# Kernel optimization log

Hardware: AMD Instinct MI355X
Metric: run time of the kernel (lower is better)

## Reference

```python
import jax, jax.numpy as jnp
import numpy as np

HID = 2048      # hidden_size
NH = 16         # num_attention_heads
QLR = 1536      # q_lora_rank
KVLR = 512      # kv_lora_rank
DN = 128        # qk_nope_head_dim
DR = 64         # qk_rope_head_dim
DQK = DN + DR   # qk_head_dim = 192
DV = 128        # v_head_dim
EPS = 1e-6
THETA = 10000.0
B, T = 2, 2048


def rmsnorm(x, scale):
    return x * jax.lax.rsqrt(jnp.mean(x * x, axis=-1, keepdims=True) + EPS) * scale


def rope(x, positions):
    # x: [B, T, h, d]; NeoX-style rotate-half RoPE on the rope slice only
    d = x.shape[-1]
    inv_freq = 1.0 / (THETA ** (jnp.arange(0, d, 2, dtype=jnp.float32) / d))
    ang = positions.astype(jnp.float32)[..., None] * inv_freq       # [B, T, d/2]
    cos = jnp.cos(ang)[:, :, None, :]
    sin = jnp.sin(ang)[:, :, None, :]
    x1, x2 = jnp.split(x, 2, axis=-1)
    return jnp.concatenate([x1 * cos - x2 * sin, x2 * cos + x1 * sin], axis=-1).astype(x.dtype)


def setup_inputs() -> dict:
    key = jax.random.key(0)
    ks = jax.random.split(key, 8)
    s = 0.02
    x = jax.random.normal(ks[0], (B, T, HID), dtype=jnp.float32)
    attention_mask = jnp.ones((B, T), dtype=bool)
    positions = jnp.broadcast_to(jnp.arange(T, dtype=jnp.int32), (B, T))
    wqa = jax.random.normal(ks[1], (HID, QLR), dtype=jnp.float32) * s
    qa_scale = jnp.ones((QLR,), dtype=jnp.float32)
    wqb = jax.random.normal(ks[2], (QLR, NH * DQK), dtype=jnp.float32) * s
    wkva = jax.random.normal(ks[3], (HID, KVLR + DR), dtype=jnp.float32) * s
    kva_scale = jnp.ones((KVLR,), dtype=jnp.float32)
    wkvb = jax.random.normal(ks[4], (KVLR, NH * (DN + DV)), dtype=jnp.float32) * s
    wo = jax.random.normal(ks[5], (NH * DV, HID), dtype=jnp.float32) * s
    return {"x": x, "attention_mask": attention_mask, "positions": positions,
            "wqa": wqa, "qa_scale": qa_scale, "wqb": wqb,
            "wkva": wkva, "kva_scale": kva_scale, "wkvb": wkvb, "wo": wo}


def reference(x, attention_mask, positions, wqa, qa_scale, wqb, wkva, kva_scale, wkvb, wo):
    Bv, Tv, _ = x.shape
    # low-rank Q: hid -> q_lora_rank -> rmsnorm -> heads*qk_head_dim
    q = (rmsnorm(x @ wqa, qa_scale) @ wqb).reshape(Bv, Tv, NH, DQK)
    q_pass, q_rot = q[..., :DN], q[..., DN:]
    # compressed KV + shared rope key
    ckv = x @ wkva                                    # [B, T, KVLR + DR]
    kv_lat, k_rot = ckv[..., :KVLR], ckv[..., KVLR:].reshape(Bv, Tv, 1, DR)
    kv = (rmsnorm(kv_lat, kva_scale) @ wkvb).reshape(Bv, Tv, NH, DN + DV)
    k_pass, v = kv[..., :DN], kv[..., DN:]
    # decoupled RoPE on rope slice only
    q_rot = rope(q_rot, positions)
    k_rot = jnp.broadcast_to(rope(k_rot, positions), (Bv, Tv, NH, DR))
    q = jnp.concatenate([q_pass, q_rot], axis=-1)     # [B, T, H, 192]
    k = jnp.concatenate([k_pass, k_rot], axis=-1)
    # masked causal SDPA; v padding in the original is a no-op mathematically
    scale = DQK ** -0.5
    scores = jnp.einsum('bqhd,bkhd->bhqk', q, k) * scale
    causal = jnp.tril(jnp.ones((Tv, Tv), dtype=bool))
    mask = causal[None, None, :, :] & attention_mask[:, None, None, :].astype(bool)
    scores = jnp.where(mask, scores, jnp.finfo(scores.dtype).min)
    probs = jax.nn.softmax(scores, axis=-1)
    out = jnp.einsum('bhqk,bkhd->bqhd', probs, v).reshape(Bv, Tv, NH * DV)
    return out @ wo
```

## Files before the change

kernel.cpp:

```cpp
#include <hip/hip_runtime.h>
#include <math.h>
#include <stdint.h>

#define NHEAD 16
#define HIDDIM 2048
#define QLRANK 1536
#define KVRANK 512
#define DROT 64
#define BB 2
#define TT 2048
#define BTOK (BB*TT)
#define NPROJ 2304
#define CKV0 1536
#define ROT0 2048

typedef __bf16 bf16x8 __attribute__((ext_vector_type(8)));
typedef __bf16 bf16x4 __attribute__((ext_vector_type(4)));
typedef float f32x4 __attribute__((ext_vector_type(4)));
typedef uint16_t u16;
typedef uint32_t u32;

__device__ __forceinline__ u16 f2bf(float f) {
  union { float f; uint32_t u; } v; v.f = f;
  uint32_t r = v.u + 0x7fffu + ((v.u >> 16) & 1u);
  return (u16)(r >> 16);
}
__device__ __forceinline__ float bf2f(u16 h) {
  union { uint32_t u; float f; } v; v.u = ((uint32_t)h) << 16;
  return v.f;
}

__device__ __forceinline__ void gload_lds16(const u16* g, u16* l) {
  __builtin_amdgcn_global_load_lds(
      (const __attribute__((address_space(1))) uint32_t*)g,
      (__attribute__((address_space(3))) uint32_t*)l, 16, 0, 0);
}

__global__ __launch_bounds__(256) void cvt_f32_bf16(const float* __restrict__ in,
                                                    u16* __restrict__ out, int n) {
  int idx = (blockIdx.x * 256 + threadIdx.x) * 8;
  if (idx >= n) return;
  f32x4 a = *(const f32x4*)&in[idx];
  f32x4 b = *(const f32x4*)&in[idx + 4];
  union { f32x4 q; u16 e[8]; } w;
#pragma unroll
  for (int j = 0; j < 4; ++j) { w.e[j] = f2bf(a[j]); w.e[4 + j] = f2bf(b[j]); }
  *(f32x4*)&out[idx] = w.q;
}

__global__ __launch_bounds__(256) void transpose_w(const float* __restrict__ W,
                                                   u16* __restrict__ Wt,
                                                   int K, int N, int Npad, float scale,
                                                   const float* __restrict__ svec) {
  __shared__ float tile[32][33];
  int k0 = blockIdx.x * 32, n0 = blockIdx.y * 32;
  int tx = threadIdx.x, ty = threadIdx.y;
#pragma unroll
  for (int r = 0; r < 32; r += 8) {
    int k = k0 + ty + r, n = n0 + tx;
    tile[ty + r][tx] = (k < K && n < N) ? W[(size_t)k * N + n] : 0.f;
  }
  __syncthreads();
  float sv = scale * (svec ? svec[k0 + tx] : 1.f);
#pragma unroll
  for (int r = 0; r < 32; r += 8) {
    int n = n0 + ty + r, k = k0 + tx;
    if (n < Npad && k < K) Wt[(size_t)n * K + k] = f2bf(tile[tx][ty + r] * sv);
  }
}

template<int D>
__global__ __launch_bounds__(256) void row_invrms(const u16* __restrict__ in, int stride,
                                                  float* __restrict__ out) {
  const int row = blockIdx.x;
  const int tid = threadIdx.x;
  constexpr int NC = D / 8;
  float ss = 0.f;
  if (tid < NC) {
    union { f32x4 q; u16 e[8]; } t;
    t.q = *(const f32x4*)&in[(size_t)row * stride + tid * 8];
#pragma unroll
    for (int j = 0; j < 8; ++j) { float v = bf2f(t.e[j]); ss += v * v; }
  }
#pragma unroll
  for (int off = 1; off < 64; off <<= 1) ss += __shfl_xor(ss, off);
  __shared__ float red[4];
  if ((tid & 63) == 0) red[tid >> 6] = ss;
  __syncthreads();
  if (tid == 0)
    out[row] = rsqrtf((red[0] + red[1] + red[2] + red[3]) / (float)D + 1e-6f);
}

template<int OUTF32>
__global__ __launch_bounds__(256) void gemm_bt(const u16* __restrict__ A, int lda,
                                               const u16* __restrict__ Bt,
                                               void* __restrict__ Cv, int ldc,
                                               const float* __restrict__ rowscale,
                                               int N, int K) {
  __shared__ __align__(16) u16 As[2][128 * 32];
  __shared__ __align__(16) u16 Bs[2][128 * 32];
  const int tid = threadIdx.x;
  const int lane = tid & 63;
  const int wave = tid >> 6;
  const int bm = blockIdx.y * 128;
  const int bn = blockIdx.x * 128;
  const int wr = wave >> 1;
  const int wc = wave & 1;

  f32x4 acc[4][4] = {};

  const int srow = wave * 16 + (lane >> 2);
  const int scol = (lane & 3) * 8;
  const u16* Ag = A + (size_t)(bm + srow) * lda + scol;
  const u16* Bg = Bt + (size_t)(bn + srow) * K + scol;
  const int soff = (wave * 16) * 32;

  const int a_off = (wr * 64 + (lane & 15)) * 32 + (lane >> 4) * 8;
  const int b_off = (wc * 64 + (lane & 15)) * 32 + (lane >> 4) * 8;

  const int nt = K >> 5;

  gload_lds16(Ag, &As[0][soff]);
  gload_lds16(Ag + (size_t)64 * lda, &As[0][soff + 64 * 32]);
  gload_lds16(Bg, &Bs[0][soff]);
  gload_lds16(Bg + (size_t)64 * K, &Bs[0][soff + 64 * 32]);
  __syncthreads();

  int cur = 0;
  for (int t = 0; t < nt; ++t) {
    if (t + 1 < nt) {
      const int k0 = (t + 1) << 5;
      gload_lds16(Ag + k0, &As[cur ^ 1][soff]);
      gload_lds16(Ag + (size_t)64 * lda + k0, &As[cur ^ 1][soff + 64 * 32]);
      gload_lds16(Bg + k0, &Bs[cur ^ 1][soff]);
      gload_lds16(Bg + (size_t)64 * K + k0, &Bs[cur ^ 1][soff + 64 * 32]);
    }
    bf16x8 af[4], bfr[4];
#pragma unroll
    for (int m = 0; m < 4; ++m) af[m] = *(const bf16x8*)&As[cur][a_off + m * 16 * 32];
#pragma unroll
    for (int n = 0; n < 4; ++n) bfr[n] = *(const bf16x8*)&Bs[cur][b_off + n * 16 * 32];
#pragma unroll
    for (int m = 0; m < 4; ++m)
#pragma unroll
      for (int n = 0; n < 4; ++n)
        acc[m][n] = __builtin_amdgcn_mfma_f32_16x16x32_bf16(af[m], bfr[n], acc[m][n], 0, 0, 0);
    if (t + 1 < nt) {
      __syncthreads();
      cur ^= 1;
    }
  }

  const int row0 = bm + wr * 64 + (lane >> 4) * 4;
  const int col0 = bn + wc * 64 + (lane & 15);
#pragma unroll
  for (int m = 0; m < 4; ++m) {
    float rs[4] = {1.f, 1.f, 1.f, 1.f};
    if (rowscale) {
#pragma unroll
      for (int i = 0; i < 4; ++i) rs[i] = rowscale[row0 + m * 16 + i];
    }
#pragma unroll
    for (int n = 0; n < 4; ++n)
#pragma unroll
      for (int i = 0; i < 4; ++i) {
        size_t idx = (size_t)(row0 + m * 16 + i) * ldc + (col0 + n * 16);
        float v = acc[m][n][i] * rs[i];
        if (OUTF32) ((float*)Cv)[idx] = v;
        else        ((u16*)Cv)[idx] = f2bf(v);
      }
  }
}

template<int OUTF32>
__global__ __launch_bounds__(512, 2) void gemm256(const u16* __restrict__ A, int lda,
                                                  const u16* __restrict__ Bt,
                                                  void* __restrict__ Cv, int ldc,
                                                  const float* __restrict__ rowscale,
                                                  int K) {
  __shared__ __align__(16) u16 S[2][2][16384];
  const int tid = threadIdx.x, lane = tid & 63, wave = tid >> 6;
  const int l15 = lane & 15, l4 = lane >> 4;
  const int bm = blockIdx.y * 256, bn = blockIdx.x * 256;
  const int wm = wave >> 2, wn = wave & 3;

  const int rlo = lane >> 3;
  const int cbase = (((lane & 7) ^ (rlo & 7)) * 8);
  const u16* src[8];
  u16* dst[8];
#pragma unroll
  for (int j = 0; j < 8; ++j) {
    int gj = wave * 8 + j;
    if (gj < 32) {
      src[j] = A + (size_t)(bm + gj * 8 + rlo) * lda + cbase;
      dst[j] = &S[0][0][0] + gj * 512;
    } else {
      src[j] = Bt + (size_t)(bn + (gj - 32) * 8 + rlo) * K + cbase;
      dst[j] = &S[0][1][0] + (gj - 32) * 512;
    }
  }

  const int r7 = l15 & 7;
  const int acol = (l4 ^ r7) * 16;
  const char* Sa0 = (const char*)&S[0][0][0] + wm * 16384;
  const char* Sb0 = (const char*)&S[0][1][0] + (wn >> 1) * 16384;
  const int arow0 = l15 * 128;
  const int brow0 = ((wn & 1) * 64 + l15) * 128;

  f32x4 acc[8][4] = {};
  const int nt = K >> 6;

#pragma unroll
  for (int j = 0; j < 8; ++j) gload_lds16(src[j], dst[j]);
#pragma unroll
  for (int j = 0; j < 8; ++j) gload_lds16(src[j] + 64, dst[j] + 32768);
  asm volatile("s_waitcnt vmcnt(8)" ::: "memory");
  __builtin_amdgcn_s_barrier();
  __builtin_amdgcn_sched_barrier(0);

  for (int t = 0; t < nt; ++t) {
    const char* Sab = Sa0 + (t & 1) * 65536;
    const char* Sbb = Sb0 + (t & 1) * 65536;
    bf16x8 bfr[4][2];
#pragma unroll
    for (int fn = 0; fn < 4; ++fn) {
      bfr[fn][0] = *(const bf16x8*)(Sbb + brow0 + fn * 2048 + acol);
      bfr[fn][1] = *(const bf16x8*)(Sbb + brow0 + fn * 2048 + (acol ^ 64));
    }
#pragma unroll
    for (int q = 0; q < 4; ++q) {
      bf16x8 a0[2], a1[2];
#pragma unroll
      for (int m2 = 0; m2 < 2; ++m2) {
        const int fm = q * 2 + m2;
        a0[m2] = *(const bf16x8*)(Sab + arow0 + fm * 2048 + acol);
        a1[m2] = *(const bf16x8*)(Sab + arow0 + fm * 2048 + (acol ^ 64));
      }
      __builtin_amdgcn_s_setprio(1);
#pragma unroll
      for (int m2 = 0; m2 < 2; ++m2)
#pragma unroll
        for (int fn = 0; fn < 4; ++fn) {
          f32x4 c = acc[q * 2 + m2][fn];
          c = __builtin_amdgcn_mfma_f32_16x16x32_bf16(a0[m2], bfr[fn][0], c, 0, 0, 0);
          c = __builtin_amdgcn_mfma_f32_16x16x32_bf16(a1[m2], bfr[fn][1], c, 0, 0, 0);
          acc[q * 2 + m2][fn] = c;
        }
      __builtin_amdgcn_s_setprio(0);
    }
    if (t + 1 < nt) {
      __builtin_amdgcn_s_barrier();
      __builtin_amdgcn_sched_barrier(0);
      if (t + 2 < nt) {
        const int koff = (t + 2) * 64;
#pragma unroll
        for (int j = 0; j < 8; ++j) gload_lds16(src[j] + koff, dst[j] + (t & 1) * 32768);
        asm volatile("s_waitcnt vmcnt(8)" ::: "memory");
      } else {
        asm volatile("s_waitcnt vmcnt(0)" ::: "memory");
      }
      __builtin_amdgcn_s_barrier();
      __builtin_amdgcn_sched_barrier(0);
    }
  }

  const int row0 = bm + wm * 128 + l4 * 4;
  const int col0 = bn + wn * 64 + l15;
#pragma unroll
  for (int fm = 0; fm < 8; ++fm) {
    float rs[4] = {1.f, 1.f, 1.f, 1.f};
    if (rowscale) {
#pragma unroll
      for (int i = 0; i < 4; ++i) rs[i] = rowscale[row0 + fm * 16 + i];
    }
#pragma unroll
    for (int fn = 0; fn < 4; ++fn)
#pragma unroll
      for (int i = 0; i < 4; ++i) {
        size_t idx = (size_t)(row0 + fm * 16 + i) * ldc + (col0 + fn * 16);
        float v = acc[fm][fn][i] * rs[i];
        if (OUTF32) ((float*)Cv)[idx] = v;
        else        ((u16*)Cv)[idx] = f2bf(v);
      }
  }
}

__global__ __launch_bounds__(256) void rope_table(const int* __restrict__ positions,
                                                  float2* __restrict__ tab) {
  int idx = blockIdx.x * 256 + threadIdx.x;
  if (idx >= BTOK * 32) return;
  int bt = idx >> 5, i = idx & 31;
  float invf = powf(10000.0f, -(float)i / 32.0f);
  float ang = (float)positions[bt] * invf;
  tab[idx] = make_float2(cosf(ang), sinf(ang));
}

__global__ __launch_bounds__(256) void rope_q(u16* __restrict__ q,
                                              const float2* __restrict__ tab) {
  int idx = blockIdx.x * 256 + threadIdx.x;
  if (idx >= BTOK * NHEAD * 32) return;
  int i = idx & 31;
  int h = (idx >> 5) & 15;
  int bt = idx >> 9;
  u16* p = q + (size_t)bt * 3072 + h * 192 + 128;
  float x1 = bf2f(p[i]), x2 = bf2f(p[32 + i]);
  float2 cs = tab[bt * 32 + i];
  p[i] = f2bf(x1 * cs.x - x2 * cs.y);
  p[32 + i] = f2bf(x2 * cs.x + x1 * cs.y);
}

__global__ __launch_bounds__(256) void assemble_k(const u16* __restrict__ kv,
                                                  const u16* __restrict__ proj,
                                                  const float2* __restrict__ tab,
                                                  u16* __restrict__ kf) {
  int bt = blockIdx.x;
  __shared__ __align__(16) u16 krot[64];
  int t = threadIdx.x;
  if (t < 64) {
    int i = t & 31;
    float2 cs = tab[bt * 32 + i];
    float x1 = bf2f(proj[(size_t)bt * NPROJ + ROT0 + i]);
    float x2 = bf2f(proj[(size_t)bt * NPROJ + ROT0 + 32 + i]);
    krot[t] = f2bf((t < 32) ? (x1 * cs.x - x2 * cs.y) : (x2 * cs.x + x1 * cs.y));
  }
  __syncthreads();
  for (int c = t; c < 16 * 24; c += 256) {
    int h = c / 24, seg = c % 24;
    u16* dst = kf + (size_t)bt * 3072 + h * 192 + seg * 8;
    if (seg < 16)
      *(f32x4*)dst = *(const f32x4*)&kv[(size_t)bt * 4096 + h * 256 + seg * 8];
    else
      *(f32x4*)dst = *(const f32x4*)&krot[(seg - 16) * 8];
  }
}

__device__ const int8_t JOB_QT[24] = {15,15,7,14,14,13,13,6,12,12,11,11,5,10,10,9,9,4,8,8,3,2,1,0};
__device__ const int8_t JOB_PC[24] = { 0, 1,2, 0, 1, 0, 1,2, 0, 1, 0, 1,2, 0, 1,0,1,2,0,1,2,2,2,2};

__global__ __launch_bounds__(256, 2) void attn_fwd6(const u16* __restrict__ Q,
                                                    const u16* __restrict__ Kf,
                                                    const u16* __restrict__ KV,
                                                    u16* __restrict__ O,
                                                    u16* __restrict__ Opart,
                                                    float2* __restrict__ ml) {
  __shared__ __align__(16) u16 Ks[64 * 192];
  __shared__ __align__(16) u16 Vs[64 * 128];
  __shared__ __align__(16) u16 Ps[4][32][72];

  const int tid = threadIdx.x, lane = tid & 63, wave = tid >> 6;
  const int l15 = lane & 15, l4 = lane >> 4;
  const int jobrank = blockIdx.x >> 5;
  const int bh = blockIdx.x & 31;
  const int qt = JOB_QT[jobrank];
  const int piece = JOB_PC[jobrank];
  const int q0 = qt * 128;
  const int b = bh >> 4, h = bh & 15;
  const int wq0 = q0 + wave * 32;

  bf16x8 qf[2][6];
#pragma unroll
  for (int m = 0; m < 2; ++m) {
    const u16* qp = Q + (size_t)(b * TT + wq0 + m * 16 + l15) * 3072 + h * 192 + l4 * 8;
#pragma unroll
    for (int kk = 0; kk < 6; ++kk) qf[m][kk] = *(const bf16x8*)(qp + kk * 32);
  }

  int ksrc[6];
#pragma unroll
  for (int j = 0; j < 6; ++j) {
    int o = (wave * 6 + j) * 1024 + lane * 16;
    int row = o / 384, col = o % 384;
    int scol = col ^ ((row & 7) << 4);
    ksrc[j] = row * 3072 + (scol >> 1);
  }
  int vsrc[4];
#pragma unroll
  for (int j = 0; j < 4; ++j) {
    int lam = (wave * 4 + j) * 512 + lane * 8;
    int kap = ((lam >> 6) & 15) * 4 + ((lam >> 4) & 3);
    int key = ((kap >> 5) & 1) * 32 + ((kap >> 2) & 3) * 8 + ((kap >> 4) & 1) * 4 + (kap & 3);
    int dv  = (lam >> 10) * 16 + (lam & 15);
    vsrc[j] = key * 4096 + dv;
  }
  const u16* Kbase = Kf + (size_t)(b * TT) * 3072 + h * 192;
  const u16* Vbase = KV + (size_t)(b * TT) * 4096 + h * 256 + 128;
  u16* KsW = Ks + (wave * 6) * 512;
  u16* VsW = Vs + (wave * 4) * 512;
  const unsigned vs_base = (unsigned)(uintptr_t)(&Vs[0]);

  f32x4 o_acc[2][8] = {};
  float m_r[2], l_r[2];
#pragma unroll
  for (int m = 0; m < 2; ++m) { m_r[m] = -INFINITY; l_r[m] = 0.f; }

  const int kt0 = (piece == 1) ? (qt + 1) : 0;
  const int kt1 = (piece == 0) ? (qt + 1) : (2 * qt + 2);

  for (int kt = kt0; kt < kt1; ++kt) {
    __syncthreads();
    const u16* Kt = Kbase + (size_t)(kt * 64) * 3072;
    const u16* Vt = Vbase + (size_t)(kt * 64) * 4096;
#pragma unroll
    for (int j = 0; j < 6; ++j) gload_lds16(Kt + ksrc[j], KsW + j * 512);
#pragma unroll
    for (int j = 0; j < 4; ++j) gload_lds16(Vt + vsrc[j], VsW + j * 512);
    __syncthreads();

    if (kt * 64 > wq0 + 31) continue;
    const int kt64 = kt * 64;

    f32x4 s[2][4] = {};
    __builtin_amdgcn_s_setprio(1);
#pragma unroll
    for (int n = 0; n < 4; ++n) {
      const int krow = n * 16 + l15;
      const int swz = (l15 & 7) << 3;
#pragma unroll
      for (int kk = 0; kk < 6; ++kk) {
        bf16x8 kb = *(const bf16x8*)&Ks[krow * 192 + ((kk * 32 + l4 * 8) ^ swz)];
        s[0][n] = __builtin_amdgcn_mfma_f32_16x16x32_bf16(kb, qf[0][kk], s[0][n], 0, 0, 0);
        s[1][n] = __builtin_amdgcn_mfma_f32_16x16x32_bf16(kb, qf[1][kk], s[1][n], 0, 0, 0);
      }
    }
    __builtin_amdgcn_s_setprio(0);

#pragma unroll
    for (int m = 0; m < 2; ++m) {
      const int qrow = wq0 + m * 16 + l15;
      const bool needmask = (kt64 + 63) > (wq0 + m * 16);
      if (needmask) {
#pragma unroll
        for (int n = 0; n < 4; ++n)
#pragma unroll
          for (int i = 0; i < 4; ++i)
            if (kt64 + n * 16 + l4 * 4 + i > qrow) s[m][n][i] = -INFINITY;
      }
      float pmax = -INFINITY;
#pragma unroll
      for (int n = 0; n < 4; ++n)
#pragma unroll
        for (int i = 0; i < 4; ++i) pmax = fmaxf(pmax, s[m][n][i]);
      pmax = fmaxf(pmax, __shfl_xor(pmax, 16));
      pmax = fmaxf(pmax, __shfl_xor(pmax, 32));

      if (!__all(pmax - m_r[m] <= 8.f)) {
        float mn = fmaxf(m_r[m], pmax);
        float alpha = __expf(m_r[m] - mn);
        m_r[m] = mn;
        l_r[m] *= alpha;
        float ab[4];
#pragma unroll
        for (int i = 0; i < 4; ++i) ab[i] = __shfl(alpha, l4 * 4 + i);
#pragma unroll
        for (int n = 0; n < 8; ++n)
#pragma unroll
          for (int i = 0; i < 4; ++i) o_acc[m][n][i] *= ab[i];
      }

      float psum = 0.f;
#pragma unroll
      for (int n = 0; n < 4; ++n) {
        float p0 = __expf(s[m][n][0] - m_r[m]);
        float p1 = __expf(s[m][n][1] - m_r[m]);
        float p2 = __expf(s[m][n][2] - m_r[m]);
        float p3 = __expf(s[m][n][3] - m_r[m]);
        psum += (p0 + p1) + (p2 + p3);
        union { uint2 d; u16 e[4]; } pw;
        pw.e[0] = f2bf(p0); pw.e[1] = f2bf(p1);
        pw.e[2] = f2bf(p2); pw.e[3] = f2bf(p3);
        *(uint2*)&Ps[wave][m * 16 + l15][n * 16 + l4 * 4] = pw.d;
      }
      psum += __shfl_xor(psum, 16);
      psum += __shfl_xor(psum, 32);
      l_r[m] += psum;
    }

    asm volatile("s_waitcnt lgkmcnt(0)" ::: "memory");
    __builtin_amdgcn_sched_barrier(0);

#pragma unroll
    for (int kk = 0; kk < 2; ++kk) {
      bf16x8 pa[2];
      pa[0] = *(const bf16x8*)&Ps[wave][l15][kk * 32 + l4 * 8];
      pa[1] = *(const bf16x8*)&Ps[wave][16 + l15][kk * 32 + l4 * 8];
      const unsigned va = vs_base + kk * 1024 + lane * 8;
#pragma unroll
      for (int g = 0; g < 2; ++g) {
        union { uint2 u; bf16x4 b; } lo[4], hi[4];
#pragma unroll
        for (int n = 0; n < 4; ++n) {
          unsigned a0 = va + (g * 4 + n) * 2048;
          asm volatile("ds_read_b64_tr_b16 %0, %1" : "=v"(lo[n].u) : "v"(a0));
          asm volatile("ds_read_b64_tr_b16 %0, %1 offset:512" : "=v"(hi[n].u) : "v"(a0));
        }
        asm volatile("s_waitcnt lgkmcnt(0)" ::: "memory");
        __builtin_amdgcn_sched_barrier(0);
        __builtin_amdgcn_s_setprio(1);
#pragma unroll
        for (int n = 0; n < 4; ++n) {
          bf16x8 vb = __builtin_shufflevector(lo[n].b, hi[n].b, 0, 1, 2, 3, 4, 5, 6, 7);
          o_acc[0][g * 4 + n] = __builtin_amdgcn_mfma_f32_16x16x32_bf16(pa[0], vb, o_acc[0][g * 4 + n], 0, 0, 0);
          o_acc[1][g * 4 + n] = __builtin_amdgcn_mfma_f32_16x16x32_bf16(pa[1], vb, o_acc[1][g * 4 + n], 0, 0, 0);
        }
        __builtin_amdgcn_s_setprio(0);
      }
    }
  }

  if (piece == 2) {
#pragma unroll
    for (int m = 0; m < 2; ++m) {
      float inv = 1.f / l_r[m];
      float li[4];
#pragma unroll
      for (int i = 0; i < 4; ++i) li[i] = __shfl(inv, l4 * 4 + i);
#pragma unroll
      for (int n = 0; n < 8; ++n)
#pragma unroll
        for (int i = 0; i < 4; ++i) {
          int r = wq0 + m * 16 + l4 * 4 + i;
          O[(size_t)(b * TT + r) * 2048 + h * 128 + n * 16 + l15] = f2bf(o_acc[m][n][i] * li[i]);
        }
    }
  } else {
    const size_t pidx = ((size_t)(qt - 8) * 32 + bh) * 2 + piece;
    u16* op = Opart + pidx * (128 * 128);
    float2* mlp = ml + pidx * 128;
#pragma unroll
    for (int m = 0; m < 2; ++m)
#pragma unroll
      for (int n = 0; n < 8; ++n)
#pragma unroll
        for (int i = 0; i < 4; ++i)
          op[(wave * 32 + m * 16 + l4 * 4 + i) * 128 + n * 16 + l15] = f2bf(o_acc[m][n][i]);
    if (l4 == 0) {
#pragma unroll
      for (int m = 0; m < 2; ++m)
        mlp[wave * 32 + m * 16 + l15] = make_float2(m_r[m], l_r[m]);
    }
  }
}

__global__ __launch_bounds__(256) void attn_combine(const u16* __restrict__ Opart,
                                                    const float2* __restrict__ ml,
                                                    u16* __restrict__ O) {
  int gid = blockIdx.x * 256 + threadIdx.x;
  int dvseg = gid & 15;
  int row = (gid >> 4) & 127;
  int bh = (gid >> 11) & 31;
  int qt8 = gid >> 16;
  size_t i1 = ((size_t)qt8 * 32 + bh) * 2;
  float2 ml1 = ml[i1 * 128 + row], ml2 = ml[(i1 + 1) * 128 + row];
  float m = fmaxf(ml1.x, ml2.x);
  float w1 = __expf(ml1.x - m), w2 = __expf(ml2.x - m);
  float inv = 1.f / (w1 * ml1.y + w2 * ml2.y);
  union { f32x4 q; u16 e[8]; } a, bq, w;
  a.q  = *(const f32x4*)&Opart[i1 * 16384 + row * 128 + dvseg * 8];
  bq.q = *(const f32x4*)&Opart[(i1 + 1) * 16384 + row * 128 + dvseg * 8];
#pragma unroll
  for (int j = 0; j < 8; ++j)
    w.e[j] = f2bf((w1 * bf2f(a.e[j]) + w2 * bf2f(bq.e[j])) * inv);
  int b = bh >> 4, h = bh & 15;
  int r = 1024 + qt8 * 128 + row;
  *(f32x4*)&O[(size_t)(b * TT + r) * 2048 + h * 128 + dvseg * 8] = w.q;
}

extern "C" void kernel_launch(void* const* d_in, const int* in_sizes, int n_in,
                              void* d_out, int out_size, void* d_ws, size_t ws_size,
                              hipStream_t stream) {
  (void)in_sizes; (void)n_in; (void)out_size; (void)ws_size;
  const float* x         = (const float*)d_in[0];
  const int*   positions = (const int*)d_in[2];
  const float* wqa       = (const float*)d_in[3];
  const float* qa_scale  = (const float*)d_in[4];
  const float* wqb       = (const float*)d_in[5];
  const float* wkva      = (const float*)d_in[6];
  const float* kva_scale = (const float*)d_in[7];
  const float* wkvb      = (const float*)d_in[8];
  const float* wo        = (const float*)d_in[9];
  float* out = (float*)d_out;

  char* wsp = (char*)d_ws;
  auto alloc = [&](size_t bytes) {
    char* p = wsp; wsp += (bytes + 255) & ~(size_t)255; return p;
  };
  u16* xb      = (u16*)alloc((size_t)BTOK * HIDDIM * 2);
  u16* proj_t  = (u16*)alloc((size_t)NPROJ * HIDDIM * 2);
  u16* wqb_t   = (u16*)alloc((size_t)3072 * QLRANK * 2);
  u16* wkvb_t  = (u16*)alloc((size_t)4096 * KVRANK * 2);
  u16* wo_t    = (u16*)alloc((size_t)HIDDIM * HIDDIM * 2);
  u16* proj    = (u16*)alloc((size_t)BTOK * NPROJ * 2);
  u16* q       = (u16*)alloc((size_t)BTOK * 3072 * 2);
  u16* kv      = (u16*)alloc((size_t)BTOK * 4096 * 2);
  u16* kf      = (u16*)alloc((size_t)BTOK * 3072 * 2);
  float2* tab  = (float2*)alloc((size_t)BTOK * 32 * 8);
  float* invq  = (float*)alloc((size_t)BTOK * 4);
  float* invkv = (float*)alloc((size_t)BTOK * 4);
  float2* mlbuf= (float2*)alloc((size_t)8 * 32 * 2 * 128 * 8);
  u16* ao = xb;
  u16* Opart = proj;

  dim3 blk(256);
  dim3 blk512(512);
  const float qscale = 0.07216878364870322f;

  cvt_f32_bf16<<<(BTOK * HIDDIM / 8 + 255) / 256, blk, 0, stream>>>(x, xb, BTOK * HIDDIM);
  {
    dim3 tb(32, 8);
    transpose_w<<<dim3(HIDDIM / 32, QLRANK / 32), tb, 0, stream>>>(wqa, proj_t, HIDDIM, QLRANK, QLRANK, 1.f, nullptr);
    transpose_w<<<dim3(HIDDIM / 32, (NPROJ - CKV0) / 32), tb, 0, stream>>>(wkva, proj_t + (size_t)CKV0 * HIDDIM, HIDDIM, 576, NPROJ - CKV0, 1.f, nullptr);
    transpose_w<<<dim3(QLRANK / 32, 3072 / 32), tb, 0, stream>>>(wqb, wqb_t, QLRANK, 3072, 3072, qscale, qa_scale);
    transpose_w<<<dim3(KVRANK / 32, 4096 / 32), tb, 0, stream>>>(wkvb, wkvb_t, KVRANK, 4096, 4096, 1.f, kva_scale);
    transpose_w<<<dim3(HIDDIM / 32, HIDDIM / 32), tb, 0, stream>>>(wo, wo_t, HIDDIM, HIDDIM, HIDDIM, 1.f, nullptr);
  }
  rope_table<<<(BTOK * 32 + 255) / 256, blk, 0, stream>>>(positions, tab);

  gemm_bt<0><<<dim3(NPROJ / 128, BTOK / 128), blk, 0, stream>>>(xb, HIDDIM, proj_t, proj, NPROJ, nullptr, NPROJ, HIDDIM);

  row_invrms<QLRANK><<<BTOK, blk, 0, stream>>>(proj, NPROJ, invq);
  row_invrms<KVRANK><<<BTOK, blk, 0, stream>>>(proj + CKV0, NPROJ, invkv);

  gemm256<0><<<dim3(3072 / 256, BTOK / 256), blk512, 0, stream>>>(proj, NPROJ, wqb_t, q, 3072, invq, QLRANK);
  gemm256<0><<<dim3(4096 / 256, BTOK / 256), blk512, 0, stream>>>(proj + CKV0, NPROJ, wkvb_t, kv, 4096, invkv, KVRANK);

  rope_q<<<(BTOK * NHEAD * 32 + 255) / 256, blk, 0, stream>>>(q, tab);
  assemble_k<<<BTOK, blk, 0, stream>>>(kv, proj, tab, kf);

  attn_fwd6<<<dim3(24 * 32), blk, 0, stream>>>(q, kf, kv, ao, Opart, mlbuf);
  attn_combine<<<(8 * 32 * 128 * 16) / 256, blk, 0, stream>>>(Opart, mlbuf, ao);

  gemm_bt<1><<<dim3(HIDDIM / 128, BTOK / 128), blk, 0, stream>>>(ao, HIDDIM, wo_t, out, HIDDIM, nullptr, HIDDIM, HIDDIM);
}
```

Baseline: 333.6 us.

## Interleave tile prefetch with MFMA phases in 256x256 bf16 GEMM

Replaces the double-buffered 256x256 GEMM with a variant that splits each K-tile's global-to-LDS loads into four quarter chunks, one issued per compute phase. The next A tile and the tile after that for B are fetched while MFMAs run. Barriers now bracket each of the four phases, and launch bounds go from 2 blocks per CU to 1. The aim is to hide load latency inside the compute loop, at the cost of more barriers per tile and possibly lower occupancy.

```diff
diff --git a/kernel.cpp b/kernel.cpp
--- a/kernel.cpp
+++ b/kernel.cpp
@@ -173,92 +173,111 @@
 }
 
 template<int OUTF32>
-__global__ __launch_bounds__(512, 2) void gemm256(const u16* __restrict__ A, int lda,
-                                                  const u16* __restrict__ Bt,
-                                                  void* __restrict__ Cv, int ldc,
-                                                  const float* __restrict__ rowscale,
-                                                  int K) {
-  __shared__ __align__(16) u16 S[2][2][16384];
+__global__ __launch_bounds__(512, 1) void gemm8p(const u16* __restrict__ A, int lda,
+                                                 const u16* __restrict__ Bt,
+                                                 void* __restrict__ Cv, int ldc,
+                                                 const float* __restrict__ rowscale,
+                                                 int K) {
+  __shared__ __align__(16) u16 S[65536];
   const int tid = threadIdx.x, lane = tid & 63, wave = tid >> 6;
   const int l15 = lane & 15, l4 = lane >> 4;
   const int bm = blockIdx.y * 256, bn = blockIdx.x * 256;
-  const int wm = wave >> 2, wn = wave & 3;
-
-  const int rlo = lane >> 3;
-  const int cbase = (((lane & 7) ^ (rlo & 7)) * 8);
-  const u16* src[8];
-  u16* dst[8];
-#pragma unroll
-  for (int j = 0; j < 8; ++j) {
-    int gj = wave * 8 + j;
-    if (gj < 32) {
-      src[j] = A + (size_t)(bm + gj * 8 + rlo) * lda + cbase;
-      dst[j] = &S[0][0][0] + gj * 512;
-    } else {
-      src[j] = Bt + (size_t)(bn + (gj - 32) * 8 + rlo) * K + cbase;
-      dst[j] = &S[0][1][0] + (gj - 32) * 512;
-    }
-  }
-
-  const int r7 = l15 & 7;
-  const int acol = (l4 ^ r7) * 16;
-  const char* Sa0 = (const char*)&S[0][0][0] + wm * 16384;
-  const char* Sb0 = (const char*)&S[0][1][0] + (wn >> 1) * 16384;
-  const int arow0 = l15 * 128;
-  const int brow0 = ((wn & 1) * 64 + l15) * 128;
+  const int wm = wave >> 2, wn = wave & 3, wh = wn >> 1;
+
+  int rowc[2], colc[2];
+#pragma unroll
+  for (int c = 0; c < 2; ++c) {
+    int o = c * 8192 + tid * 16;
+    int row = o >> 7;
+    int slot = (o >> 4) & 7;
+    rowc[c] = row;
+    colc[c] = (slot ^ (row & 7)) * 8;
+  }
+  const u16* pa[2][2];
+  const u16* pb[2][2];
+#pragma unroll
+  for (int h = 0; h < 2; ++h)
+#pragma unroll
+    for (int c = 0; c < 2; ++c) {
+      pa[h][c] = A  + (size_t)(bm + h * 128 + rowc[c]) * lda + colc[c];
+      pb[h][c] = Bt + (size_t)(bn + h * 128 + rowc[c]) * K   + colc[c];
+    }
+  auto stA = [&](int h, int t) {
+    u16* d = &S[(((t & 1) * 2 + 0) * 2 + h) * 8192 + tid * 8];
+    gload_lds16(pa[h][0] + t * 64, d);
+    gload_lds16(pa[h][1] + t * 64, d + 4096);
+  };
+  auto stB = [&](int h, int t) {
+    u16* d = &S[(((t & 1) * 2 + 1) * 2 + h) * 8192 + tid * 8];
+    gload_lds16(pb[h][0] + t * 64, d);
+    gload_lds16(pb[h][1] + t * 64, d + 4096);
+  };
+
+  const char* Sc = (const char*)S;
+  const int sw = l15 & 7;
+  const int sl0 = ((0 + l4) ^ sw) * 16;
+  const int sl1 = ((4 + l4) ^ sw) * 16;
+  const int aoff = (0 * 2 + wm) * 16384 + l15 * 128;
+  const int boff = (1 * 2 + wh) * 16384 + ((wn & 1) * 64 + l15) * 128;
 
   f32x4 acc[8][4] = {};
   const int nt = K >> 6;
 
-#pragma unroll
-  for (int j = 0; j < 8; ++j) gload_lds16(src[j], dst[j]);
-#pragma unroll
-  for (int j = 0; j < 8; ++j) gload_lds16(src[j] + 64, dst[j] + 32768);
-  asm volatile("s_waitcnt vmcnt(8)" ::: "memory");
+  stA(0, 0); stA(1, 0); stB(0, 0); stB(1, 0);
+  if (nt > 1) {
+    stB(0, 1); stB(1, 1);
+    asm volatile("s_waitcnt vmcnt(4)" ::: "memory");
+  } else {
+    asm volatile("s_waitcnt vmcnt(0)" ::: "memory");
+  }
   __builtin_amdgcn_s_barrier();
   __builtin_amdgcn_sched_barrier(0);
 
   for (int t = 0; t < nt; ++t) {
-    const char* Sab = Sa0 + (t & 1) * 65536;
-    const char* Sbb = Sb0 + (t & 1) * 65536;
+    const int buf = (t & 1) * 65536;
     bf16x8 bfr[4][2];
 #pragma unroll
-    for (int fn = 0; fn < 4; ++fn) {
-      bfr[fn][0] = *(const bf16x8*)(Sbb + brow0 + fn * 2048 + acol);
-      bfr[fn][1] = *(const bf16x8*)(Sbb + brow0 + fn * 2048 + (acol ^ 64));
-    }
-#pragma unroll
     for (int q = 0; q < 4; ++q) {
-      bf16x8 a0[2], a1[2];
+      bf16x8 afr[2][2];
 #pragma unroll
       for (int m2 = 0; m2 < 2; ++m2) {
-        const int fm = q * 2 + m2;
-        a0[m2] = *(const bf16x8*)(Sab + arow0 + fm * 2048 + acol);
-        a1[m2] = *(const bf16x8*)(Sab + arow0 + fm * 2048 + (acol ^ 64));
-      }
+        const int fo = buf + aoff + (2 * q + m2) * 2048;
+        afr[m2][0] = *(const bf16x8*)(Sc + fo + sl0);
+        afr[m2][1] = *(const bf16x8*)(Sc + fo + sl1);
+      }
+      if (q == 0) {
+#pragma unroll
+        for (int fn = 0; fn < 4; ++fn) {
+          const int fo = buf + boff + fn * 2048;
+          bfr[fn][0] = *(const bf16x8*)(Sc + fo + sl0);
+          bfr[fn][1] = *(const bf16x8*)(Sc + fo + sl1);
+        }
+      }
+      if (q == 0)      { if (t + 1 < nt) stA(0, t + 1); }
+      else if (q == 1) { if (t + 1 < nt) stA(1, t + 1); }
+      else if (q == 2) { if (t + 2 < nt) stB(0, t + 2); }
+      else             { if (t + 2 < nt) stB(1, t + 2); }
+
+      __builtin_amdgcn_s_barrier();
+      asm volatile("s_waitcnt lgkmcnt(0)" ::: "memory");
+      __builtin_amdgcn_sched_barrier(0);
       __builtin_amdgcn_s_setprio(1);
 #pragma unroll
       for (int m2 = 0; m2 < 2; ++m2)
 #pragma unroll
         for (int fn = 0; fn < 4; ++fn) {
-          f32x4 c = acc[q * 2 + m2][fn];
-          c = __builtin_amdgcn_mfma_f32_16x16x32_bf16(a0[m2], bfr[fn][0], c, 0, 0, 0);
-          c = __builtin_amdgcn_mfma_f32_16x16x32_bf16(a1[m2], bfr[fn][1], c, 0, 0, 0);
-          acc[q * 2 + m2][fn] = c;
+          f32x4 c = acc[2 * q + m2][fn];
+          c = __builtin_amdgcn_mfma_f32_16x16x32_bf16(afr[m2][0], bfr[fn][0], c, 0, 0, 0);
+          c = __builtin_amdgcn_mfma_f32_16x16x32_bf16(afr[m2][1], bfr[fn][1], c, 0, 0, 0);
+          acc[2 * q + m2][fn] = c;
         }
       __builtin_amdgcn_s_setprio(0);
-    }
-    if (t + 1 < nt) {
       __builtin_amdgcn_s_barrier();
       __builtin_amdgcn_sched_barrier(0);
-      if (t + 2 < nt) {
-        const int koff = (t + 2) * 64;
-#pragma unroll
-        for (int j = 0; j < 8; ++j) gload_lds16(src[j] + koff, dst[j] + (t & 1) * 32768);
-        asm volatile("s_waitcnt vmcnt(8)" ::: "memory");
-      } else {
-        asm volatile("s_waitcnt vmcnt(0)" ::: "memory");
-      }
+    }
+    if (t + 1 < nt) {
+      if (t + 2 < nt) asm volatile("s_waitcnt vmcnt(4)" ::: "memory");
+      else            asm volatile("s_waitcnt vmcnt(0)" ::: "memory");
       __builtin_amdgcn_s_barrier();
       __builtin_amdgcn_sched_barrier(0);
     }
@@ -620,8 +639,8 @@
   row_invrms<QLRANK><<<BTOK, blk, 0, stream>>>(proj, NPROJ, invq);
   row_invrms<KVRANK><<<BTOK, blk, 0, stream>>>(proj + CKV0, NPROJ, invkv);
 
-  gemm256<0><<<dim3(3072 / 256, BTOK / 256), blk512, 0, stream>>>(proj, NPROJ, wqb_t, q, 3072, invq, QLRANK);
-  gemm256<0><<<dim3(4096 / 256, BTOK / 256), blk512, 0, stream>>>(proj + CKV0, NPROJ, wkvb_t, kv, 4096, invkv, KVRANK);
+  gemm8p<0><<<dim3(3072 / 256, BTOK / 256), blk512, 0, stream>>>(proj, NPROJ, wqb_t, q, 3072, invq, QLRANK);
+  gemm8p<0><<<dim3(4096 / 256, BTOK / 256), blk512, 0, stream>>>(proj + CKV0, NPROJ, wkvb_t, kv, 4096, invkv, KVRANK);
 
   rope_q<<<(BTOK * NHEAD * 32 + 255) / 256, blk, 0, stream>>>(q, tab);
   assemble_k<<<BTOK, blk, 0, stream>>>(kv, proj, tab, kf);
```

Measured after the change: 327.5 us. About the same (-1.8%).
